# Kernel optimization log

Hardware: AMD Instinct MI355X
Metric: run time of the kernel (lower is better)

Reference implementation:

```python
import jax, jax.numpy as jnp
import numpy as np

N_NODES = 100000
N_EDGES = 3200000
F_IN, F_HID, F_OUT = 36, 8, 2
NEG_SLOPE = 0.2


def gat_layer(x, src, dst, W, a_src, a_dst, b, num_nodes):
    # Linear transform: [N, F'] 
    h = x @ W
    # Per-node attention logits (heads=1)
    alpha_s = h @ a_src  # [N]
    alpha_d = h @ a_dst  # [N]
    # Edge-wise score: leaky_relu(a_src . h_j + a_dst . h_i) for edge j->i
    e = jax.nn.leaky_relu(alpha_s[src] + alpha_d[dst], negative_slope=NEG_SLOPE)  # [E]
    # Segment softmax over incoming edges of each dst node
    m = jax.ops.segment_max(e, dst, num_segments=num_nodes)  # [N]
    ee = jnp.exp(e - m[dst])
    denom = jax.ops.segment_sum(ee, dst, num_segments=num_nodes)  # [N]
    alpha = ee / denom[dst]  # [E]
    # Scatter-aggregate messages
    out = jax.ops.segment_sum(alpha[:, None] * h[src], dst, num_segments=num_nodes)
    return out + b


def setup_inputs() -> dict:
    key = jax.random.key(0)
    ks = jax.random.split(key, 10)
    x = jax.random.normal(ks[0], (N_NODES, F_IN), dtype=jnp.float32)
    edge_index = jax.random.randint(ks[1], (2, N_EDGES), 0, N_NODES, dtype=jnp.int64)
    s1 = 1.0 / np.sqrt(F_IN)
    s2 = 1.0 / np.sqrt(F_HID)
    W1 = jax.random.uniform(ks[2], (F_IN, F_HID), jnp.float32, -s1, s1)
    a_src1 = jax.random.uniform(ks[3], (F_HID,), jnp.float32, -s2, s2)
    a_dst1 = jax.random.uniform(ks[4], (F_HID,), jnp.float32, -s2, s2)
    b1 = jnp.zeros((F_HID,), jnp.float32)
    W2 = jax.random.uniform(ks[5], (F_HID, F_OUT), jnp.float32, -s2, s2)
    so = 1.0 / np.sqrt(F_OUT)
    a_src2 = jax.random.uniform(ks[6], (F_OUT,), jnp.float32, -so, so)
    a_dst2 = jax.random.uniform(ks[7], (F_OUT,), jnp.float32, -so, so)
    b2 = jnp.zeros((F_OUT,), jnp.float32)
    return {"x": x, "edge_index": edge_index, "W1": W1, "a_src1": a_src1,
            "a_dst1": a_dst1, "b1": b1, "W2": W2, "a_src2": a_src2,
            "a_dst2": a_dst2, "b2": b2}


def reference(x, edge_index, W1, a_src1, a_dst1, b1, W2, a_src2, a_dst2, b2):
    src, dst = edge_index[0], edge_index[1]
    n = x.shape[0]
    h = jax.nn.relu(gat_layer(x, src, dst, W1, a_src1, a_dst1, b1, n))
    # dropout is identity in eval mode
    out = gat_layer(h, src, dst, W2, a_src2, a_dst2, b2, n)
    return jax.nn.log_softmax(out, axis=1)
```

## Files before the change

kernel.cpp:

```cpp
#include <hip/hip_runtime.h>
#include <hip/hip_bf16.h>

#define N_NODES 100000
#define N_EDGES 3200000
#define F_IN 36
#define F_HID 8
#define F_OUT 2
#define NEG_SLOPE 0.2f

#define SHIFT_C 10
#define NCB 98
#define CAPC 36000
#define GSHIFT 7
#define GNPB 128
#define GNBUCK 782
#define CAPF 4480
#define NB_PART 256
#define CHUNK 12500
#define BP 1024
#define BP2 512
#define BPG 512

__device__ __forceinline__ int detect_is64(const void* eidx, int* s_flag) {
    if (threadIdx.x < 64) {
        const unsigned int* p = (const unsigned int*)eidx;
        unsigned int v1 = p[2 * threadIdx.x + 1];
        unsigned int v2 = p[2 * (threadIdx.x + 64) + 1];
        unsigned long long m = __ballot(v1 != 0u || v2 != 0u);
        if (threadIdx.x == 0) *s_flag = (m == 0ull) ? 1 : 0;
    }
    __syncthreads();
    return *s_flag;
}

__global__ void part1_k(const void* __restrict__ eidx, int* __restrict__ gcnt_c,
                        int* __restrict__ partC) {
    __shared__ int h[NCB];
    __shared__ int s_flag;
    int t = threadIdx.x;
    if (t < NCB) h[t] = 0;
    int f = detect_is64(eidx, &s_flag);
    int beg = blockIdx.x * CHUNK;
    int end = beg + CHUNK; if (end > N_EDGES) end = N_EDGES;
    if (f) {
        const long long* p = (const long long*)eidx;
        for (int i = beg + t; i < end; i += BP) atomicAdd(&h[(int)p[N_EDGES + i] >> SHIFT_C], 1);
    } else {
        const int* p = (const int*)eidx;
        for (int i = beg + t; i < end; i += BP) atomicAdd(&h[p[N_EDGES + i] >> SHIFT_C], 1);
    }
    __syncthreads();
    if (t < NCB) {
        int c = h[t];
        h[t] = c ? atomicAdd(&gcnt_c[t], c) : 0;
    }
    __syncthreads();
    if (f) {
        const long long* p = (const long long*)eidx;
        for (int i = beg + t; i < end; i += BP) {
            int s = (int)p[i];
            int d = (int)p[N_EDGES + i];
            int b = d >> SHIFT_C;
            int pos = atomicAdd(&h[b], 1);
            if (pos < CAPC) partC[b * CAPC + pos] = (s << SHIFT_C) | (d & 1023);
        }
    } else {
        const int* p = (const int*)eidx;
        for (int i = beg + t; i < end; i += BP) {
            int s = p[i];
            int d = p[N_EDGES + i];
            int b = d >> SHIFT_C;
            int pos = atomicAdd(&h[b], 1);
            if (pos < CAPC) partC[b * CAPC + pos] = (s << SHIFT_C) | (d & 1023);
        }
    }
}

__global__ void part2_k(const int* __restrict__ gcnt_c, const int* __restrict__ partC,
                        int* __restrict__ gcnt_f, int* __restrict__ fineP) {
    __shared__ int h8[8];
    __shared__ int cur8[8];
    int t = threadIdx.x;
    int cb = blockIdx.x >> 3;
    int k = blockIdx.x & 7;
    int cntc = gcnt_c[cb]; if (cntc > CAPC) cntc = CAPC;
    int sbeg = (int)((long long)k * cntc / 8);
    int send = (int)((long long)(k + 1) * cntc / 8);
    const int* cp = partC + (size_t)cb * CAPC;

    if (t < 8) h8[t] = 0;
    __syncthreads();
    for (int j = sbeg + t; j < send; j += BP2)
        atomicAdd(&h8[(cp[j] >> GSHIFT) & 7], 1);
    __syncthreads();
    if (t < 8) {
        int c = h8[t];
        cur8[t] = c ? atomicAdd(&gcnt_f[cb * 8 + t], c) : 0;
    }
    __syncthreads();
    for (int j = sbeg + t; j < send; j += BP2) {
        int pk = cp[j];
        int fidx = (pk >> GSHIFT) & 7;
        int pos = atomicAdd(&cur8[fidx], 1);
        if (pos < CAPF)
            fineP[(size_t)(cb * 8 + fidx) * CAPF + pos] =
                ((pk >> SHIFT_C) << GSHIFT) | (pk & (GNPB - 1));
    }
}

__global__ void node1_k(const float* __restrict__ x, const float* __restrict__ W1,
                        const float* __restrict__ aw_s, const float* __restrict__ aw_d,
                        float* __restrict__ h1, float* __restrict__ as1, float* __restrict__ ad1,
                        int n_nodes) {
    int n = blockIdx.x * blockDim.x + threadIdx.x;
    if (n >= n_nodes) return;
    float acc[F_HID];
#pragma unroll
    for (int f = 0; f < F_HID; f++) acc[f] = 0.f;
    const float4* xp = (const float4*)(x + (size_t)n * F_IN);
#pragma unroll
    for (int q = 0; q < 9; q++) {
        float4 xv = xp[q];
        const float* w = W1 + q * 4 * F_HID;
#pragma unroll
        for (int f = 0; f < F_HID; f++) {
            acc[f] += xv.x * w[0 * F_HID + f] + xv.y * w[1 * F_HID + f]
                    + xv.z * w[2 * F_HID + f] + xv.w * w[3 * F_HID + f];
        }
    }
    float s = 0.f, d = 0.f;
#pragma unroll
    for (int f = 0; f < F_HID; f++) {
        s += acc[f] * aw_s[f];
        d += acc[f] * aw_d[f];
    }
    float4* hp = (float4*)(h1 + (size_t)n * F_HID);
    hp[0] = make_float4(acc[0], acc[1], acc[2], acc[3]);
    hp[1] = make_float4(acc[4], acc[5], acc[6], acc[7]);
    as1[n] = s;
    ad1[n] = d;
}

__global__ void gatF1_k(const int* __restrict__ gcnt_f, const int* __restrict__ fineP,
                        int* __restrict__ e_srcP, int2* __restrict__ rowinfo,
                        const float* __restrict__ as1, const float* __restrict__ ad1,
                        const float* __restrict__ h1, const float* __restrict__ b1,
                        const float* __restrict__ W2, const float* __restrict__ aw_s2,
                        const float* __restrict__ aw_d2, float4* __restrict__ P2) {
    __shared__ int eL[CAPF];
    __shared__ int hist[GNPB];
    __shared__ int nstart[GNPB];
    __shared__ int cursor[GNPB];
    __shared__ int sscan[GNPB];
    __shared__ float adl[GNPB];
    int t = threadIdx.x;
    int c = blockIdx.x;
    int nbase = c << GSHIFT;
    size_t beg = (size_t)c * CAPF;
    int cnt = gcnt_f[c]; if (cnt > CAPF) cnt = CAPF;

    if (t < GNPB) {
        hist[t] = 0;
        adl[t] = (nbase + t < N_NODES) ? ad1[nbase + t] : 0.f;
    }
    __syncthreads();
    for (int j = t; j < cnt; j += BPG)
        atomicAdd(&hist[fineP[beg + j] & (GNPB - 1)], 1);
    __syncthreads();
    if (t < GNPB) sscan[t] = hist[t];
    __syncthreads();
    for (int o = 1; o < GNPB; o <<= 1) {
        int u = (t < GNPB && t >= o) ? sscan[t - o] : 0;
        __syncthreads();
        if (t < GNPB) sscan[t] += u;
        __syncthreads();
    }
    if (t < GNPB) {
        int ex = sscan[t] - hist[t];
        nstart[t] = ex;
        cursor[t] = ex;
        int node = nbase + t;
        if (node < N_NODES) rowinfo[node] = make_int2((int)beg + ex, hist[t]);
    }
    __syncthreads();
    for (int j = t; j < cnt; j += BPG) {
        int pk = fineP[beg + j];
        int pos = atomicAdd(&cursor[pk & (GNPB - 1)], 1);
        eL[pos] = pk >> GSHIFT;
    }
    __syncthreads();
    for (int i = t; i < cnt; i += BPG) e_srcP[beg + i] = eL[i];

    int node = t >> 2;
    int lane = t & 3;
    int gnode = nbase + node;
    if (gnode >= N_NODES) return;
    int ns = nstart[node];
    int ne = ns + hist[node];
    float add = adl[node];

    float denom = 0.f;
    float acc[F_HID];
#pragma unroll
    for (int f = 0; f < F_HID; f++) acc[f] = 0.f;
    for (int i = ns + lane; i < ne; i += 4) {
        int s = eL[i];
        float e = as1[s] + add;
        e = e >= 0.f ? e : NEG_SLOPE * e;
        float ee = __expf(e);
        denom += ee;
        const float4* hp = (const float4*)(h1 + (size_t)s * F_HID);
        float4 p0 = hp[0], p1 = hp[1];
        acc[0] += ee * p0.x; acc[1] += ee * p0.y; acc[2] += ee * p0.z; acc[3] += ee * p0.w;
        acc[4] += ee * p1.x; acc[5] += ee * p1.y; acc[6] += ee * p1.z; acc[7] += ee * p1.w;
    }
#pragma unroll
    for (int o = 2; o > 0; o >>= 1) {
        denom += __shfl_xor(denom, o, 4);
#pragma unroll
        for (int f = 0; f < F_HID; f++) acc[f] += __shfl_xor(acc[f], o, 4);
    }
    if (lane == 0) {
        float inv = denom > 0.f ? 1.f / denom : 0.f;
        float o0 = 0.f, o1 = 0.f;
#pragma unroll
        for (int f = 0; f < F_HID; f++) {
            float v = acc[f] * inv + b1[f];
            v = v > 0.f ? v : 0.f;
            o0 += v * W2[f * F_OUT + 0];
            o1 += v * W2[f * F_OUT + 1];
        }
        float as2v = o0 * aw_s2[0] + o1 * aw_s2[1];
        float ad2v = o0 * aw_d2[0] + o1 * aw_d2[1];
        P2[gnode] = make_float4(as2v, o0, o1, ad2v);
    }
}

__global__ void gat2_k(const int2* __restrict__ rowinfo, const int* __restrict__ e_srcP,
                       const float4* __restrict__ P2, const float* __restrict__ b2,
                       float* __restrict__ out, int n_nodes) {
    int gid = blockIdx.x * 16 + (threadIdx.x >> 4);
    int lane = threadIdx.x & 15;
    if (gid >= n_nodes) return;
    int2 ri = rowinfo[gid];
    float add = P2[gid].w;

    float denom = 0.f, a0 = 0.f, a1 = 0.f;
    int jend = ri.x + ri.y;
    for (int j = ri.x + lane; j < jend; j += 16) {
        int s = e_srcP[j];
        float4 q = P2[s];
        float e = q.x + add;
        e = e >= 0.f ? e : NEG_SLOPE * e;
        float ee = __expf(e);
        denom += ee;
        a0 += ee * q.y;
        a1 += ee * q.z;
    }
#pragma unroll
    for (int o = 8; o > 0; o >>= 1) {
        denom += __shfl_xor(denom, o, 16);
        a0 += __shfl_xor(a0, o, 16);
        a1 += __shfl_xor(a1, o, 16);
    }

    if (lane == 0) {
        float inv = denom > 0.f ? 1.f / denom : 0.f;
        float o0 = a0 * inv + b2[0];
        float o1 = a1 * inv + b2[1];
        float M = fmaxf(o0, o1);
        float l = M + logf(__expf(o0 - M) + __expf(o1 - M));
        ((float2*)out)[gid] = make_float2(o0 - l, o1 - l);
    }
}

extern "C" void kernel_launch(void* const* d_in, const int* in_sizes, int n_in,
                              void* d_out, int out_size, void* d_ws, size_t ws_size,
                              hipStream_t stream) {
    const float* x      = (const float*)d_in[0];
    const void*  eidx   = d_in[1];
    const float* W1     = (const float*)d_in[2];
    const float* a_src1 = (const float*)d_in[3];
    const float* a_dst1 = (const float*)d_in[4];
    const float* b1     = (const float*)d_in[5];
    const float* W2     = (const float*)d_in[6];
    const float* a_src2 = (const float*)d_in[7];
    const float* a_dst2 = (const float*)d_in[8];
    const float* b2     = (const float*)d_in[9];
    float* out = (float*)d_out;

    const size_t N = N_NODES;
    const size_t SZC = (size_t)NCB * CAPC;
    const size_t SZF = (size_t)784 * CAPF;

    int* wsi = (int*)d_ws;
    float* wsf = (float*)d_ws;
    size_t o = 0;
    int* partC    = wsi + o;      o += SZC;
    int* e_srcP   = partC;
    int* fineP    = wsi + o;      o += SZF;
    int* gcnt_c   = wsi + o;      o += 128;
    int* gcnt_f   = wsi + o;      o += 800;
    int2* rowinfo = (int2*)(wsi + o); o += 2 * N;
    float* as1    = wsf + o;      o += N;
    float* ad1    = wsf + o;      o += N;
    float* h1     = wsf + o;      o += 8 * N;
    float4* P2    = (float4*)(wsf + o); o += 4 * N;

    const int B = 256;
    const int gridN = (int)((N + B - 1) / B);
    const int gridG = (int)(N / 16);

    hipMemsetAsync(gcnt_c, 0, (128 + 800) * sizeof(int), stream);

    part1_k<<<NB_PART, BP, 0, stream>>>(eidx, gcnt_c, partC);
    part2_k<<<NCB * 8, BP2, 0, stream>>>(gcnt_c, partC, gcnt_f, fineP);
    node1_k<<<gridN, B, 0, stream>>>(x, W1, a_src1, a_dst1, h1, as1, ad1, (int)N);
    gatF1_k<<<GNBUCK, BPG, 0, stream>>>(gcnt_f, fineP, e_srcP, rowinfo, as1, ad1, h1, b1,
                                        W2, a_src2, a_dst2, P2);
    gat2_k<<<gridG, B, 0, stream>>>(rowinfo, e_srcP, P2, b2, out, (int)N);
}
```

Before: 191.7 us.

## Fuse node transform into partition kernel and halve fine bucket size

Merges the per-node linear transform into the edge-partition kernel as extra blocks, so one launch runs both and they overlap. Fine buckets shrink from 128 to 64 nodes, which doubles the second-level split to 16 ways and launches 1568 smaller gatF1 blocks of 256 threads. e_srcP gets its own workspace instead of aliasing partC. The goal is better occupancy and load balance in gatF1 and less launch and serialization overhead, at the cost of more buckets, more global atomics and a larger workspace.

```diff
diff --git a/kernel.cpp b/kernel.cpp
--- a/kernel.cpp
+++ b/kernel.cpp
@@ -11,15 +11,15 @@
 #define SHIFT_C 10
 #define NCB 98
 #define CAPC 36000
-#define GSHIFT 7
-#define GNPB 128
-#define GNBUCK 782
-#define CAPF 4480
+#define GSHIFT 6
+#define GNPB 64
+#define NFINE 1568
+#define CAPF 2368
 #define NB_PART 256
 #define CHUNK 12500
 #define BP 1024
 #define BP2 512
-#define BPG 512
+#define BPG 256
 
 __device__ __forceinline__ int detect_is64(const void* eidx, int* s_flag) {
     if (threadIdx.x < 64) {
@@ -33,11 +33,45 @@
     return *s_flag;
 }
 
-__global__ void part1_k(const void* __restrict__ eidx, int* __restrict__ gcnt_c,
-                        int* __restrict__ partC) {
+__global__ void part1_node1_k(const void* __restrict__ eidx, int* __restrict__ gcnt_c,
+                              int* __restrict__ partC,
+                              const float* __restrict__ x, const float* __restrict__ W1,
+                              const float* __restrict__ aw_s, const float* __restrict__ aw_d,
+                              float* __restrict__ h1, float* __restrict__ as1,
+                              float* __restrict__ ad1) {
+    int t = threadIdx.x;
+    if (blockIdx.x >= NB_PART) {
+        int n = (blockIdx.x - NB_PART) * BP + t;
+        if (n >= N_NODES) return;
+        float acc[F_HID];
+#pragma unroll
+        for (int f = 0; f < F_HID; f++) acc[f] = 0.f;
+        const float4* xp = (const float4*)(x + (size_t)n * F_IN);
+#pragma unroll
+        for (int q = 0; q < 9; q++) {
+            float4 xv = xp[q];
+            const float* w = W1 + q * 4 * F_HID;
+#pragma unroll
+            for (int f = 0; f < F_HID; f++) {
+                acc[f] += xv.x * w[0 * F_HID + f] + xv.y * w[1 * F_HID + f]
+                        + xv.z * w[2 * F_HID + f] + xv.w * w[3 * F_HID + f];
+            }
+        }
+        float s = 0.f, d = 0.f;
+#pragma unroll
+        for (int f = 0; f < F_HID; f++) {
+            s += acc[f] * aw_s[f];
+            d += acc[f] * aw_d[f];
+        }
+        float4* hp = (float4*)(h1 + (size_t)n * F_HID);
+        hp[0] = make_float4(acc[0], acc[1], acc[2], acc[3]);
+        hp[1] = make_float4(acc[4], acc[5], acc[6], acc[7]);
+        as1[n] = s;
+        ad1[n] = d;
+        return;
+    }
     __shared__ int h[NCB];
     __shared__ int s_flag;
-    int t = threadIdx.x;
     if (t < NCB) h[t] = 0;
     int f = detect_is64(eidx, &s_flag);
     int beg = blockIdx.x * CHUNK;
@@ -78,8 +112,8 @@
 
 __global__ void part2_k(const int* __restrict__ gcnt_c, const int* __restrict__ partC,
                         int* __restrict__ gcnt_f, int* __restrict__ fineP) {
-    __shared__ int h8[8];
-    __shared__ int cur8[8];
+    __shared__ int h16[16];
+    __shared__ int cur16[16];
     int t = threadIdx.x;
     int cb = blockIdx.x >> 3;
     int k = blockIdx.x & 7;
@@ -88,57 +122,24 @@
     int send = (int)((long long)(k + 1) * cntc / 8);
     const int* cp = partC + (size_t)cb * CAPC;
 
-    if (t < 8) h8[t] = 0;
+    if (t < 16) h16[t] = 0;
     __syncthreads();
     for (int j = sbeg + t; j < send; j += BP2)
-        atomicAdd(&h8[(cp[j] >> GSHIFT) & 7], 1);
-    __syncthreads();
-    if (t < 8) {
-        int c = h8[t];
-        cur8[t] = c ? atomicAdd(&gcnt_f[cb * 8 + t], c) : 0;
+        atomicAdd(&h16[(cp[j] >> GSHIFT) & 15], 1);
+    __syncthreads();
+    if (t < 16) {
+        int c = h16[t];
+        cur16[t] = c ? atomicAdd(&gcnt_f[cb * 16 + t], c) : 0;
     }
     __syncthreads();
     for (int j = sbeg + t; j < send; j += BP2) {
         int pk = cp[j];
-        int fidx = (pk >> GSHIFT) & 7;
-        int pos = atomicAdd(&cur8[fidx], 1);
+        int fidx = (pk >> GSHIFT) & 15;
+        int pos = atomicAdd(&cur16[fidx], 1);
         if (pos < CAPF)
-            fineP[(size_t)(cb * 8 + fidx) * CAPF + pos] =
+            fineP[(size_t)(cb * 16 + fidx) * CAPF + pos] =
                 ((pk >> SHIFT_C) << GSHIFT) | (pk & (GNPB - 1));
     }
-}
-
-__global__ void node1_k(const float* __restrict__ x, const float* __restrict__ W1,
-                        const float* __restrict__ aw_s, const float* __restrict__ aw_d,
-                        float* __restrict__ h1, float* __restrict__ as1, float* __restrict__ ad1,
-                        int n_nodes) {
-    int n = blockIdx.x * blockDim.x + threadIdx.x;
-    if (n >= n_nodes) return;
-    float acc[F_HID];
-#pragma unroll
-    for (int f = 0; f < F_HID; f++) acc[f] = 0.f;
-    const float4* xp = (const float4*)(x + (size_t)n * F_IN);
-#pragma unroll
-    for (int q = 0; q < 9; q++) {
-        float4 xv = xp[q];
-        const float* w = W1 + q * 4 * F_HID;
-#pragma unroll
-        for (int f = 0; f < F_HID; f++) {
-            acc[f] += xv.x * w[0 * F_HID + f] + xv.y * w[1 * F_HID + f]
-                    + xv.z * w[2 * F_HID + f] + xv.w * w[3 * F_HID + f];
-        }
-    }
-    float s = 0.f, d = 0.f;
-#pragma unroll
-    for (int f = 0; f < F_HID; f++) {
-        s += acc[f] * aw_s[f];
-        d += acc[f] * aw_d[f];
-    }
-    float4* hp = (float4*)(h1 + (size_t)n * F_HID);
-    hp[0] = make_float4(acc[0], acc[1], acc[2], acc[3]);
-    hp[1] = make_float4(acc[4], acc[5], acc[6], acc[7]);
-    as1[n] = s;
-    ad1[n] = d;
 }
 
 __global__ void gatF1_k(const int* __restrict__ gcnt_f, const int* __restrict__ fineP,
@@ -291,16 +292,16 @@
 
     const size_t N = N_NODES;
     const size_t SZC = (size_t)NCB * CAPC;
-    const size_t SZF = (size_t)784 * CAPF;
+    const size_t SZF = (size_t)NFINE * CAPF;
 
     int* wsi = (int*)d_ws;
     float* wsf = (float*)d_ws;
     size_t o = 0;
     int* partC    = wsi + o;      o += SZC;
-    int* e_srcP   = partC;
     int* fineP    = wsi + o;      o += SZF;
+    int* e_srcP   = wsi + o;      o += SZF;
     int* gcnt_c   = wsi + o;      o += 128;
-    int* gcnt_f   = wsi + o;      o += 800;
+    int* gcnt_f   = wsi + o;      o += 1600;
     int2* rowinfo = (int2*)(wsi + o); o += 2 * N;
     float* as1    = wsf + o;      o += N;
     float* ad1    = wsf + o;      o += N;
@@ -308,15 +309,15 @@
     float4* P2    = (float4*)(wsf + o); o += 4 * N;
 
     const int B = 256;
-    const int gridN = (int)((N + B - 1) / B);
     const int gridG = (int)(N / 16);
-
-    hipMemsetAsync(gcnt_c, 0, (128 + 800) * sizeof(int), stream);
-
-    part1_k<<<NB_PART, BP, 0, stream>>>(eidx, gcnt_c, partC);
+    const int NODE_BLKS = (int)((N + BP - 1) / BP);
+
+    hipMemsetAsync(gcnt_c, 0, (128 + 1600) * sizeof(int), stream);
+
+    part1_node1_k<<<NB_PART + NODE_BLKS, BP, 0, stream>>>(
+        eidx, gcnt_c, partC, x, W1, a_src1, a_dst1, h1, as1, ad1);
     part2_k<<<NCB * 8, BP2, 0, stream>>>(gcnt_c, partC, gcnt_f, fineP);
-    node1_k<<<gridN, B, 0, stream>>>(x, W1, a_src1, a_dst1, h1, as1, ad1, (int)N);
-    gatF1_k<<<GNBUCK, BPG, 0, stream>>>(gcnt_f, fineP, e_srcP, rowinfo, as1, ad1, h1, b1,
-                                        W2, a_src2, a_dst2, P2);
+    gatF1_k<<<NFINE, BPG, 0, stream>>>(gcnt_f, fineP, e_srcP, rowinfo, as1, ad1, h1, b1,
+                                       W2, a_src2, a_dst2, P2);
     gat2_k<<<gridG, B, 0, stream>>>(rowinfo, e_srcP, P2, b2, out, (int)N);
 }
```

New measurement: 189.4 us. About the same (-1.2%).
